# Kernel optimization log

Measured on AMD Instinct MI355X. Metric: run time of the kernel, lower is better.

Reference implementation:

```python
import jax, jax.numpy as jnp
import numpy as np

# tiny-cuda-nn HashGrid config from the module
N_LEVELS = 12
F_PER_LEVEL = 2
LOG2_T = 16
T = 1 << LOG2_T            # 65536 entries per level
BASE_RES = 4
PER_LEVEL_SCALE = 1.61
HASH_PRIME_Y = np.uint32(2654435761)
HIDDEN = 256
OUT = 3
N_POINTS = 1048576

# per-level scale / resolution (tcnn: scale = base*s^l - 1, res = ceil(scale)+1)
_LEVEL_SCALES = [BASE_RES * (PER_LEVEL_SCALE ** l) - 1.0 for l in range(N_LEVELS)]
_LEVEL_RES = [int(np.ceil(s)) + 1 for s in _LEVEL_SCALES]

_CORNERS = np.array([[0, 0], [1, 0], [0, 1], [1, 1]], dtype=np.uint32)  # [4,2]


def hash_encode(x, tables):
    """x: [N,2] in [0,1); tables: [L,T,F]. Returns [N, L*F]."""
    offs_u = jnp.asarray(_CORNERS)                      # [4,2] uint32
    offs_f = offs_u.astype(x.dtype)                     # [4,2]
    feats = []
    for l in range(N_LEVELS):
        s = _LEVEL_SCALES[l]
        res = _LEVEL_RES[l]
        pos = x * jnp.asarray(s, x.dtype) + 0.5         # [N,2]
        p0f = jnp.floor(pos)
        w = pos - p0f                                   # [N,2] frac, differentiable
        p0 = p0f.astype(jnp.uint32)                     # [N,2]
        c = p0[:, None, :] + offs_u[None]               # [N,4,2] corner coords
        # bilinear weight per corner: prod over dims of (w if offset==1 else 1-w)
        wc = jnp.where(offs_f[None] == 1.0, w[:, None, :], 1.0 - w[:, None, :]).prod(-1)  # [N,4]
        if res * res <= T:
            # dense (tight grid) indexing
            cx = jnp.minimum(c[..., 0], np.uint32(res - 1))
            cy = jnp.minimum(c[..., 1], np.uint32(res - 1))
            idx = cx + cy * np.uint32(res)
        else:
            # spatial hash: x*1 XOR y*prime, masked to table size
            idx = (c[..., 0] ^ (c[..., 1] * HASH_PRIME_Y)) & np.uint32(T - 1)
        f = tables[l][idx.astype(jnp.int32)]            # [N,4,F] gather
        feats.append((wc[..., None] * f).sum(axis=1))   # [N,F]
    return jnp.concatenate(feats, axis=-1)              # [N, L*F]


def setup_inputs() -> dict:
    key = jax.random.key(0)
    ks = jax.random.split(key, 10)
    x = jax.random.uniform(ks[0], (N_POINTS, 2), dtype=jnp.float32)
    # tcnn initializes hash tables uniform in [-1e-4, 1e-4]
    tables = jax.random.uniform(ks[1], (N_LEVELS, T, F_PER_LEVEL), dtype=jnp.float32,
                                minval=-1e-4, maxval=1e-4)
    d_in = N_LEVELS * F_PER_LEVEL

    def lin(k, fan_in, fan_out):
        bound = 1.0 / np.sqrt(fan_in)
        kw, kb = jax.random.split(k)
        W = jax.random.uniform(kw, (fan_in, fan_out), dtype=jnp.float32, minval=-bound, maxval=bound)
        b = jax.random.uniform(kb, (fan_out,), dtype=jnp.float32, minval=-bound, maxval=bound)
        return W, b

    W1, b1 = lin(ks[2], d_in, HIDDEN)
    W2, b2 = lin(ks[3], HIDDEN, HIDDEN)
    W3, b3 = lin(ks[4], HIDDEN, HIDDEN)
    Wo, bo = lin(ks[5], HIDDEN, OUT)
    return {"x": x, "tables": tables, "W1": W1, "b1": b1, "W2": W2, "b2": b2,
            "W3": W3, "b3": b3, "Wo": Wo, "bo": bo}


def reference(x, tables, W1, b1, W2, b2, W3, b3, Wo, bo):
    enc = hash_encode(x, tables)                        # [N,24]
    h = jax.nn.relu(enc @ W1 + b1)
    h = jax.nn.relu(h @ W2 + b2)
    h = jax.nn.relu(h @ W3 + b3)
    return h @ Wo + bo                                  # [N,3]
```

## Files before the change

kernel.cpp:

```cpp
#include <hip/hip_runtime.h>

typedef _Float16 f16;
typedef _Float16 f16x2 __attribute__((ext_vector_type(2)));
typedef _Float16 f16x4 __attribute__((ext_vector_type(4)));
typedef _Float16 f16x8 __attribute__((ext_vector_type(8)));
typedef float    f32x4 __attribute__((ext_vector_type(4)));

#define ES 40
#define NPTS 128

__device__ __forceinline__ f16* hswz(f16* base, int p, int fbyte) {
  return (f16*)((char*)base + p * 512 + (fbyte ^ ((p & 7) << 4)));
}
__device__ __forceinline__ const f16* hswz(const f16* base, int p, int fbyte) {
  return (const f16*)((const char*)base + p * 512 + (fbyte ^ ((p & 7) << 4)));
}

static __device__ const float c_scale[12] = {
  3.0f, 5.44f, 9.3684f, 15.693124f, 25.87592964f, 42.2702467204f,
  68.665097219844f, 111.16080652394884f, 179.5788985035576f,
  289.7320265907278f, 467.0785628110717f, 752.6064861258255f };
static __device__ const unsigned c_res[12] = {4,7,11,17,27,44,70,113,181,291,469,754};

__global__ __launch_bounds__(256) void prep_weights(
    const float* __restrict__ W1, const float* __restrict__ W2,
    const float* __restrict__ W3, const float* __restrict__ Wo,
    f16* __restrict__ ws)
{
  int i = blockIdx.x * 256 + threadIdx.x;
  if (i < 8192) {
    int o = i >> 5, k = i & 31;
    ws[i] = (k < 24) ? (f16)W1[k * 256 + o] : (f16)0.0f;
  } else if (i < 73728) {
    int j = i - 8192; int o = j >> 8, k = j & 255;
    ws[i] = (f16)W2[k * 256 + o];
  } else if (i < 139264) {
    int j = i - 73728; int o = j >> 8, k = j & 255;
    ws[i] = (f16)W3[k * 256 + o];
  } else if (i < 143360) {
    int j = i - 139264; int o = j >> 8, k = j & 255;
    ws[i] = (o < 3) ? (f16)Wo[k * 3 + o] : (f16)0.0f;
  }
}

__device__ __forceinline__ void layer256(
    f16* h, const f16* __restrict__ WT,
    const float* __restrict__ bias,
    int w, int l15, int g)
{
  f32x4 acc[4][8];
  #pragma unroll
  for (int mt = 0; mt < 4; ++mt)
    #pragma unroll
    for (int nt = 0; nt < 8; ++nt) acc[mt][nt] = (f32x4)0.0f;

  #pragma unroll
  for (int ks = 0; ks < 8; ++ks) {
    f16x8 a[4], b[8];
    #pragma unroll
    for (int mt = 0; mt < 4; ++mt)
      a[mt] = *(const f16x8*)(WT + (w*64 + mt*16 + l15) * 256 + ks*32 + g*8);
    #pragma unroll
    for (int nt = 0; nt < 8; ++nt)
      b[nt] = *(const f16x8*)hswz(h, nt*16 + l15, ks*64 + g*16);
    #pragma unroll
    for (int mt = 0; mt < 4; ++mt)
      #pragma unroll
      for (int nt = 0; nt < 8; ++nt)
        acc[mt][nt] = __builtin_amdgcn_mfma_f32_16x16x32_f16(a[mt], b[nt], acc[mt][nt], 0, 0, 0);
  }
  __syncthreads();
  #pragma unroll
  for (int mt = 0; mt < 4; ++mt) {
    f32x4 bv = *(const f32x4*)(bias + w*64 + mt*16 + g*4);
    #pragma unroll
    for (int nt = 0; nt < 8; ++nt) {
      f16x4 hv;
      #pragma unroll
      for (int r = 0; r < 4; ++r) {
        float v = acc[mt][nt][r] + bv[r];
        hv[r] = (f16)fmaxf(v, 0.0f);
      }
      *(f16x4*)hswz(h, nt*16 + l15, (w*64 + mt*16 + g*4) * 2) = hv;
    }
  }
  __syncthreads();
}

__global__ __launch_bounds__(256, 2) void hashmlp_kernel(
    const float* __restrict__ x, const float* __restrict__ tables,
    const float* __restrict__ b1, const float* __restrict__ b2,
    const float* __restrict__ b3, const float* __restrict__ bo,
    const f16* __restrict__ ws, float* __restrict__ out)
{
  __shared__ __align__(16) f16 s_enc[NPTS * ES];
  __shared__ __align__(16) f16 s_h[NPTS * 256];

  const int tid = threadIdx.x;
  const int blk = blockIdx.x;

  {
    int p = tid >> 1, sub = tid & 1;
    int gp = blk * NPTS + p;
    float2 xy = ((const float2*)x)[gp];
    #pragma unroll
    for (int j = 0; j < 6; ++j) {
      int l = sub * 6 + j;
      float s = c_scale[l];
      unsigned res = c_res[l];
      float px = __fadd_rn(__fmul_rn(xy.x, s), 0.5f);
      float py = __fadd_rn(__fmul_rn(xy.y, s), 0.5f);
      float fx = floorf(px), fy = floorf(py);
      float wx = px - fx, wy = py - fy;
      unsigned ix = (unsigned)fx, iy = (unsigned)fy;
      unsigned i00, i10, i01, i11;
      if (res * res <= 65536u) {
        unsigned rm = res - 1u;
        unsigned x0 = min(ix, rm), x1 = min(ix + 1u, rm);
        unsigned y0 = min(iy, rm), y1 = min(iy + 1u, rm);
        i00 = x0 + y0 * res; i10 = x1 + y0 * res;
        i01 = x0 + y1 * res; i11 = x1 + y1 * res;
      } else {
        unsigned h0 = iy * 2654435761u, h1 = (iy + 1u) * 2654435761u;
        i00 = (ix ^ h0) & 65535u;  i10 = ((ix + 1u) ^ h0) & 65535u;
        i01 = (ix ^ h1) & 65535u;  i11 = ((ix + 1u) ^ h1) & 65535u;
      }
      const float2* tb = (const float2*)(tables + l * 131072);
      float2 f00 = tb[i00], f10 = tb[i10], f01 = tb[i01], f11 = tb[i11];
      float w00 = (1.f - wx) * (1.f - wy), w10 = wx * (1.f - wy);
      float w01 = (1.f - wx) * wy,         w11 = wx * wy;
      float e0 = w00 * f00.x + w10 * f10.x + w01 * f01.x + w11 * f11.x;
      float e1 = w00 * f00.y + w10 * f10.y + w01 * f01.y + w11 * f11.y;
      f16x2 pk; pk[0] = (f16)e0; pk[1] = (f16)e1;
      *(f16x2*)(&s_enc[p * ES + l * 2]) = pk;
    }
    f16x4 z; z[0] = (f16)0.0f; z[1] = (f16)0.0f; z[2] = (f16)0.0f; z[3] = (f16)0.0f;
    *(f16x4*)(&s_enc[p * ES + 24 + sub * 4]) = z;
  }
  __syncthreads();

  const int w = tid >> 6, lane = tid & 63;
  const int l15 = lane & 15, g = lane >> 4;
  const f16* W1T = ws;
  const f16* W2T = ws + 8192;
  const f16* W3T = ws + 73728;
  const f16* WoT = ws + 139264;

  {
    f32x4 acc[4][8];
    #pragma unroll
    for (int mt = 0; mt < 4; ++mt)
      #pragma unroll
      for (int nt = 0; nt < 8; ++nt) acc[mt][nt] = (f32x4)0.0f;
    f16x8 a[4], b[8];
    #pragma unroll
    for (int mt = 0; mt < 4; ++mt)
      a[mt] = *(const f16x8*)(W1T + (w*64 + mt*16 + l15) * 32 + g*8);
    #pragma unroll
    for (int nt = 0; nt < 8; ++nt)
      b[nt] = *(const f16x8*)(&s_enc[(nt*16 + l15) * ES + g*8]);
    #pragma unroll
    for (int mt = 0; mt < 4; ++mt)
      #pragma unroll
      for (int nt = 0; nt < 8; ++nt)
        acc[mt][nt] = __builtin_amdgcn_mfma_f32_16x16x32_f16(a[mt], b[nt], acc[mt][nt], 0, 0, 0);
    #pragma unroll
    for (int mt = 0; mt < 4; ++mt) {
      f32x4 bv = *(const f32x4*)(b1 + w*64 + mt*16 + g*4);
      #pragma unroll
      for (int nt = 0; nt < 8; ++nt) {
        f16x4 hv;
        #pragma unroll
        for (int r = 0; r < 4; ++r) {
          float v = acc[mt][nt][r] + bv[r];
          hv[r] = (f16)fmaxf(v, 0.0f);
        }
        *(f16x4*)hswz(s_h, nt*16 + l15, (w*64 + mt*16 + g*4) * 2) = hv;
      }
    }
  }
  __syncthreads();

  layer256(s_h, W2T, b2, w, l15, g);
  layer256(s_h, W3T, b3, w, l15, g);

  {
    f32x4 acc0 = (f32x4)0.0f, acc1 = (f32x4)0.0f;
    #pragma unroll
    for (int ks = 0; ks < 8; ++ks) {
      f16x8 a = *(const f16x8*)(WoT + l15 * 256 + ks*32 + g*8);
      f16x8 b0 = *(const f16x8*)hswz(s_h, (2*w+0)*16 + l15, ks*64 + g*16);
      f16x8 b1v = *(const f16x8*)hswz(s_h, (2*w+1)*16 + l15, ks*64 + g*16);
      acc0 = __builtin_amdgcn_mfma_f32_16x16x32_f16(a, b0, acc0, 0, 0, 0);
      acc1 = __builtin_amdgcn_mfma_f32_16x16x32_f16(a, b1v, acc1, 0, 0, 0);
    }
    if (g == 0) {
      int gp0 = blk * NPTS + (2*w+0) * 16 + l15;
      int gp1 = blk * NPTS + (2*w+1) * 16 + l15;
      out[gp0 * 3 + 0] = acc0[0] + bo[0];
      out[gp0 * 3 + 1] = acc0[1] + bo[1];
      out[gp0 * 3 + 2] = acc0[2] + bo[2];
      out[gp1 * 3 + 0] = acc1[0] + bo[0];
      out[gp1 * 3 + 1] = acc1[1] + bo[1];
      out[gp1 * 3 + 2] = acc1[2] + bo[2];
    }
  }
}

extern "C" void kernel_launch(void* const* d_in, const int* in_sizes, int n_in,
                              void* d_out, int out_size, void* d_ws, size_t ws_size,
                              hipStream_t stream) {
  const float* x  = (const float*)d_in[0];
  const float* tb = (const float*)d_in[1];
  const float* W1 = (const float*)d_in[2];
  const float* b1 = (const float*)d_in[3];
  const float* W2 = (const float*)d_in[4];
  const float* b2 = (const float*)d_in[5];
  const float* W3 = (const float*)d_in[6];
  const float* b3 = (const float*)d_in[7];
  const float* Wo = (const float*)d_in[8];
  const float* bo = (const float*)d_in[9];
  f16* ws = (f16*)d_ws;

  prep_weights<<<560, 256, 0, stream>>>(W1, W2, W3, Wo, ws);
  hashmlp_kernel<<<8192, 256, 0, stream>>>(x, tb, b1, b2, b3, bo, ws, (float*)d_out);
}
```

Before: 367.6 us.

## Use two waves per block with 128-row output tiles and bias-initialized accumulators

Cuts the block from 256 to 128 threads (2 waves), so each wave now computes 128 output neurons across 128 points. Each B fragment read from shared memory feeds twice as many MFMAs, which lowers LDS traffic per flop. Bias is folded into the accumulator initialisation, and each thread now encodes all 12 hash levels for one point. The cost is 256 fp32 accumulator registers per thread and half as many waves per CU, which risks spills and less latency hiding for the hash gathers.

```diff
diff --git a/kernel.cpp b/kernel.cpp
--- a/kernel.cpp
+++ b/kernel.cpp
@@ -48,46 +48,45 @@
     const float* __restrict__ bias,
     int w, int l15, int g)
 {
-  f32x4 acc[4][8];
+  f32x4 acc[8][8];
   #pragma unroll
-  for (int mt = 0; mt < 4; ++mt)
-    #pragma unroll
-    for (int nt = 0; nt < 8; ++nt) acc[mt][nt] = (f32x4)0.0f;
+  for (int mt = 0; mt < 8; ++mt) {
+    f32x4 bv = *(const f32x4*)(bias + w*128 + mt*16 + g*4);
+    #pragma unroll
+    for (int nt = 0; nt < 8; ++nt) acc[mt][nt] = bv;
+  }
 
   #pragma unroll
   for (int ks = 0; ks < 8; ++ks) {
-    f16x8 a[4], b[8];
-    #pragma unroll
-    for (int mt = 0; mt < 4; ++mt)
-      a[mt] = *(const f16x8*)(WT + (w*64 + mt*16 + l15) * 256 + ks*32 + g*8);
+    f16x8 a[8], b[8];
+    #pragma unroll
+    for (int mt = 0; mt < 8; ++mt)
+      a[mt] = *(const f16x8*)(WT + (w*128 + mt*16 + l15) * 256 + ks*32 + g*8);
     #pragma unroll
     for (int nt = 0; nt < 8; ++nt)
       b[nt] = *(const f16x8*)hswz(h, nt*16 + l15, ks*64 + g*16);
     #pragma unroll
-    for (int mt = 0; mt < 4; ++mt)
+    for (int mt = 0; mt < 8; ++mt)
       #pragma unroll
       for (int nt = 0; nt < 8; ++nt)
         acc[mt][nt] = __builtin_amdgcn_mfma_f32_16x16x32_f16(a[mt], b[nt], acc[mt][nt], 0, 0, 0);
   }
   __syncthreads();
   #pragma unroll
-  for (int mt = 0; mt < 4; ++mt) {
-    f32x4 bv = *(const f32x4*)(bias + w*64 + mt*16 + g*4);
+  for (int mt = 0; mt < 8; ++mt) {
     #pragma unroll
     for (int nt = 0; nt < 8; ++nt) {
       f16x4 hv;
       #pragma unroll
-      for (int r = 0; r < 4; ++r) {
-        float v = acc[mt][nt][r] + bv[r];
-        hv[r] = (f16)fmaxf(v, 0.0f);
-      }
-      *(f16x4*)hswz(h, nt*16 + l15, (w*64 + mt*16 + g*4) * 2) = hv;
-    }
-  }
-  __syncthreads();
-}
-
-__global__ __launch_bounds__(256, 2) void hashmlp_kernel(
+      for (int r = 0; r < 4; ++r)
+        hv[r] = (f16)fmaxf(acc[mt][nt][r], 0.0f);
+      *(f16x4*)hswz(h, nt*16 + l15, (w*128 + mt*16 + g*4) * 2) = hv;
+    }
+  }
+  __syncthreads();
+}
+
+__global__ __launch_bounds__(128, 1) void hashmlp_kernel(
     const float* __restrict__ x, const float* __restrict__ tables,
     const float* __restrict__ b1, const float* __restrict__ b2,
     const float* __restrict__ b3, const float* __restrict__ bo,
@@ -100,12 +99,11 @@
   const int blk = blockIdx.x;
 
   {
-    int p = tid >> 1, sub = tid & 1;
+    int p = tid;
     int gp = blk * NPTS + p;
     float2 xy = ((const float2*)x)[gp];
     #pragma unroll
-    for (int j = 0; j < 6; ++j) {
-      int l = sub * 6 + j;
+    for (int l = 0; l < 12; ++l) {
       float s = c_scale[l];
       unsigned res = c_res[l];
       float px = __fadd_rn(__fmul_rn(xy.x, s), 0.5f);
@@ -135,7 +133,8 @@
       *(f16x2*)(&s_enc[p * ES + l * 2]) = pk;
     }
     f16x4 z; z[0] = (f16)0.0f; z[1] = (f16)0.0f; z[2] = (f16)0.0f; z[3] = (f16)0.0f;
-    *(f16x4*)(&s_enc[p * ES + 24 + sub * 4]) = z;
+    *(f16x4*)(&s_enc[p * ES + 24]) = z;
+    *(f16x4*)(&s_enc[p * ES + 28]) = z;
   }
   __syncthreads();
 
@@ -147,35 +146,34 @@
   const f16* WoT = ws + 139264;
 
   {
-    f32x4 acc[4][8];
-    #pragma unroll
-    for (int mt = 0; mt < 4; ++mt)
-      #pragma unroll
-      for (int nt = 0; nt < 8; ++nt) acc[mt][nt] = (f32x4)0.0f;
-    f16x8 a[4], b[8];
-    #pragma unroll
-    for (int mt = 0; mt < 4; ++mt)
-      a[mt] = *(const f16x8*)(W1T + (w*64 + mt*16 + l15) * 32 + g*8);
+    f32x4 acc[8][8];
+    #pragma unroll
+    for (int mt = 0; mt < 8; ++mt) {
+      f32x4 bv = *(const f32x4*)(b1 + w*128 + mt*16 + g*4);
+      #pragma unroll
+      for (int nt = 0; nt < 8; ++nt) acc[mt][nt] = bv;
+    }
+    f16x8 a[8], b[8];
+    #pragma unroll
+    for (int mt = 0; mt < 8; ++mt)
+      a[mt] = *(const f16x8*)(W1T + (w*128 + mt*16 + l15) * 32 + g*8);
     #pragma unroll
     for (int nt = 0; nt < 8; ++nt)
       b[nt] = *(const f16x8*)(&s_enc[(nt*16 + l15) * ES + g*8]);
     #pragma unroll
-    for (int mt = 0; mt < 4; ++mt)
+    for (int mt = 0; mt < 8; ++mt)
       #pragma unroll
       for (int nt = 0; nt < 8; ++nt)
         acc[mt][nt] = __builtin_amdgcn_mfma_f32_16x16x32_f16(a[mt], b[nt], acc[mt][nt], 0, 0, 0);
     #pragma unroll
-    for (int mt = 0; mt < 4; ++mt) {
-      f32x4 bv = *(const f32x4*)(b1 + w*64 + mt*16 + g*4);
+    for (int mt = 0; mt < 8; ++mt) {
       #pragma unroll
       for (int nt = 0; nt < 8; ++nt) {
         f16x4 hv;
         #pragma unroll
-        for (int r = 0; r < 4; ++r) {
-          float v = acc[mt][nt][r] + bv[r];
-          hv[r] = (f16)fmaxf(v, 0.0f);
-        }
-        *(f16x4*)hswz(s_h, nt*16 + l15, (w*64 + mt*16 + g*4) * 2) = hv;
+        for (int r = 0; r < 4; ++r)
+          hv[r] = (f16)fmaxf(acc[mt][nt][r], 0.0f);
+        *(f16x4*)hswz(s_h, nt*16 + l15, (w*128 + mt*16 + g*4) * 2) = hv;
       }
     }
   }
@@ -185,24 +183,26 @@
   layer256(s_h, W3T, b3, w, l15, g);
 
   {
-    f32x4 acc0 = (f32x4)0.0f, acc1 = (f32x4)0.0f;
+    f32x4 acc[4];
+    #pragma unroll
+    for (int q = 0; q < 4; ++q) acc[q] = (f32x4)0.0f;
     #pragma unroll
     for (int ks = 0; ks < 8; ++ks) {
       f16x8 a = *(const f16x8*)(WoT + l15 * 256 + ks*32 + g*8);
-      f16x8 b0 = *(const f16x8*)hswz(s_h, (2*w+0)*16 + l15, ks*64 + g*16);
-      f16x8 b1v = *(const f16x8*)hswz(s_h, (2*w+1)*16 + l15, ks*64 + g*16);
-      acc0 = __builtin_amdgcn_mfma_f32_16x16x32_f16(a, b0, acc0, 0, 0, 0);
-      acc1 = __builtin_amdgcn_mfma_f32_16x16x32_f16(a, b1v, acc1, 0, 0, 0);
+      #pragma unroll
+      for (int q = 0; q < 4; ++q) {
+        f16x8 b = *(const f16x8*)hswz(s_h, (w*4+q)*16 + l15, ks*64 + g*16);
+        acc[q] = __builtin_amdgcn_mfma_f32_16x16x32_f16(a, b, acc[q], 0, 0, 0);
+      }
     }
     if (g == 0) {
-      int gp0 = blk * NPTS + (2*w+0) * 16 + l15;
-      int gp1 = blk * NPTS + (2*w+1) * 16 + l15;
-      out[gp0 * 3 + 0] = acc0[0] + bo[0];
-      out[gp0 * 3 + 1] = acc0[1] + bo[1];
-      out[gp0 * 3 + 2] = acc0[2] + bo[2];
-      out[gp1 * 3 + 0] = acc1[0] + bo[0];
-      out[gp1 * 3 + 1] = acc1[1] + bo[1];
-      out[gp1 * 3 + 2] = acc1[2] + bo[2];
+      #pragma unroll
+      for (int q = 0; q < 4; ++q) {
+        int gp = blk * NPTS + (w*4+q) * 16 + l15;
+        out[gp * 3 + 0] = acc[q][0] + bo[0];
+        out[gp * 3 + 1] = acc[q][1] + bo[1];
+        out[gp * 3 + 2] = acc[q][2] + bo[2];
+      }
     }
   }
 }
@@ -223,5 +223,5 @@
   f16* ws = (f16*)d_ws;
 
   prep_weights<<<560, 256, 0, stream>>>(W1, W2, W3, Wo, ws);
-  hashmlp_kernel<<<8192, 256, 0, stream>>>(x, tb, b1, b2, b3, bo, ws, (float*)d_out);
-}
+  hashmlp_kernel<<<8192, 128, 0, stream>>>(x, tb, b1, b2, b3, bo, ws, (float*)d_out);
+}
```

Result: slower. 437.7 us (+19.1%).

## Software-pipeline weight loads across MLP layers and fold bias into accumulators

Applied to the files above, without the earlier changes.

Restructures the MLP layers so global weight fragments are prefetched one to two k-steps ahead through a triple-buffered register ring. The first k-slices of the next layer's weights (and the output layer's weights) are loaded during the tail of the current layer. Bias is loaded up front and used as the initial accumulator value, and the swizzled LDS addresses are precomputed once per thread. This is meant to hide global/L2 latency of weight loads behind MFMA work, at the cost of more live registers, which could spill or reduce occupancy at the 2-block launch bound.

```diff
diff --git a/kernel.cpp b/kernel.cpp
--- a/kernel.cpp
+++ b/kernel.cpp
@@ -9,12 +9,6 @@
 #define ES 40
 #define NPTS 128
 
-__device__ __forceinline__ f16* hswz(f16* base, int p, int fbyte) {
-  return (f16*)((char*)base + p * 512 + (fbyte ^ ((p & 7) << 4)));
-}
-__device__ __forceinline__ const f16* hswz(const f16* base, int p, int fbyte) {
-  return (const f16*)((const char*)base + p * 512 + (fbyte ^ ((p & 7) << 4)));
-}
 
 static __device__ const float c_scale[12] = {
   3.0f, 5.44f, 9.3684f, 15.693124f, 25.87592964f, 42.2702467204f,
@@ -43,45 +37,73 @@
   }
 }
 
-__device__ __forceinline__ void layer256(
-    f16* h, const f16* __restrict__ WT,
-    const float* __restrict__ bias,
-    int w, int l15, int g)
+template<bool NEXT_OUT>
+__device__ __forceinline__ void layer256_pipe(
+    f16* __restrict__ h, const f16* __restrict__ WT,
+    const f32x4* bv, f16x8* cur0, f16x8* cur1,
+    const f16* __restrict__ WTn, const float* __restrict__ bn,
+    f16x8* nxt0, f16x8* nxt1, f32x4* bvn, f16x8* aout,
+    const int* vbase, const int* wbase, int w, int l15, int g)
 {
   f32x4 acc[4][8];
   #pragma unroll
   for (int mt = 0; mt < 4; ++mt)
     #pragma unroll
-    for (int nt = 0; nt < 8; ++nt) acc[mt][nt] = (f32x4)0.0f;
-
+    for (int nt = 0; nt < 8; ++nt) acc[mt][nt] = bv[mt];
+
+  f16x8 abuf[3][4];
+  #pragma unroll
+  for (int mt = 0; mt < 4; ++mt) { abuf[0][mt] = cur0[mt]; abuf[1][mt] = cur1[mt]; }
+
+  const char* hb = (const char*)h;
   #pragma unroll
   for (int ks = 0; ks < 8; ++ks) {
-    f16x8 a[4], b[8];
-    #pragma unroll
-    for (int mt = 0; mt < 4; ++mt)
-      a[mt] = *(const f16x8*)(WT + (w*64 + mt*16 + l15) * 256 + ks*32 + g*8);
-    #pragma unroll
-    for (int nt = 0; nt < 8; ++nt)
-      b[nt] = *(const f16x8*)hswz(h, nt*16 + l15, ks*64 + g*16);
-    #pragma unroll
-    for (int mt = 0; mt < 4; ++mt)
-      #pragma unroll
-      for (int nt = 0; nt < 8; ++nt)
-        acc[mt][nt] = __builtin_amdgcn_mfma_f32_16x16x32_f16(a[mt], b[nt], acc[mt][nt], 0, 0, 0);
+    if (ks < 6) {
+      #pragma unroll
+      for (int mt = 0; mt < 4; ++mt)
+        abuf[(ks+2)%3][mt] = *(const f16x8*)(WT + (w*64 + mt*16 + l15)*256 + (ks+2)*32 + g*8);
+    } else if (ks == 6) {
+      if (NEXT_OUT) {
+        #pragma unroll
+        for (int q = 0; q < 4; ++q)
+          aout[q] = *(const f16x8*)(WTn + l15*256 + q*32 + g*8);
+      } else {
+        #pragma unroll
+        for (int mt = 0; mt < 4; ++mt)
+          nxt0[mt] = *(const f16x8*)(WTn + (w*64 + mt*16 + l15)*256 + g*8);
+        #pragma unroll
+        for (int mt = 0; mt < 4; ++mt)
+          bvn[mt] = *(const f32x4*)(bn + w*64 + mt*16 + g*4);
+      }
+    } else {
+      if (NEXT_OUT) {
+        #pragma unroll
+        for (int q = 0; q < 4; ++q)
+          aout[4+q] = *(const f16x8*)(WTn + l15*256 + (4+q)*32 + g*8);
+      } else {
+        #pragma unroll
+        for (int mt = 0; mt < 4; ++mt)
+          nxt1[mt] = *(const f16x8*)(WTn + (w*64 + mt*16 + l15)*256 + 32 + g*8);
+      }
+    }
+    #pragma unroll
+    for (int nt = 0; nt < 8; ++nt) {
+      f16x8 b = *(const f16x8*)(hb + vbase[ks] + nt*8192);
+      #pragma unroll
+      for (int mt = 0; mt < 4; ++mt)
+        acc[mt][nt] = __builtin_amdgcn_mfma_f32_16x16x32_f16(abuf[ks%3][mt], b, acc[mt][nt], 0, 0, 0);
+    }
   }
   __syncthreads();
   #pragma unroll
   for (int mt = 0; mt < 4; ++mt) {
-    f32x4 bv = *(const f32x4*)(bias + w*64 + mt*16 + g*4);
     #pragma unroll
     for (int nt = 0; nt < 8; ++nt) {
       f16x4 hv;
       #pragma unroll
-      for (int r = 0; r < 4; ++r) {
-        float v = acc[mt][nt][r] + bv[r];
-        hv[r] = (f16)fmaxf(v, 0.0f);
-      }
-      *(f16x4*)hswz(h, nt*16 + l15, (w*64 + mt*16 + g*4) * 2) = hv;
+      for (int r = 0; r < 4; ++r)
+        hv[r] = (f16)fmaxf(acc[mt][nt][r], 0.0f);
+      *(f16x4*)((char*)h + wbase[mt] + nt*8192) = hv;
     }
   }
   __syncthreads();
@@ -98,6 +120,36 @@
 
   const int tid = threadIdx.x;
   const int blk = blockIdx.x;
+  const int w = tid >> 6, lane = tid & 63;
+  const int l15 = lane & 15, g = lane >> 4;
+
+  const f16* W1T = ws;
+  const f16* W2T = ws + 8192;
+  const f16* W3T = ws + 73728;
+  const f16* WoT = ws + 139264;
+
+  f16x8 a1[4], pn0[4], pn1[4];
+  f32x4 bvA[4], bvB[4];
+  #pragma unroll
+  for (int mt = 0; mt < 4; ++mt) {
+    a1[mt]  = *(const f16x8*)(W1T + (w*64 + mt*16 + l15)*32 + g*8);
+    pn0[mt] = *(const f16x8*)(W2T + (w*64 + mt*16 + l15)*256 + g*8);
+    pn1[mt] = *(const f16x8*)(W2T + (w*64 + mt*16 + l15)*256 + 32 + g*8);
+    bvA[mt] = *(const f32x4*)(b1 + w*64 + mt*16 + g*4);
+    bvB[mt] = *(const f32x4*)(b2 + w*64 + mt*16 + g*4);
+  }
+  float bo0 = bo[0], bo1 = bo[1], bo2 = bo[2];
+
+  int vbase[8], wbase[4];
+  {
+    int K = (l15 & 7) << 4;
+    #pragma unroll
+    for (int ks = 0; ks < 8; ++ks)
+      vbase[ks] = l15*512 + ((ks*64 + g*16) ^ K);
+    #pragma unroll
+    for (int mt = 0; mt < 4; ++mt)
+      wbase[mt] = l15*512 + (((w*64 + mt*16 + g*4)*2) ^ K);
+  }
 
   {
     int p = tid >> 1, sub = tid & 1;
@@ -139,70 +191,59 @@
   }
   __syncthreads();
 
-  const int w = tid >> 6, lane = tid & 63;
-  const int l15 = lane & 15, g = lane >> 4;
-  const f16* W1T = ws;
-  const f16* W2T = ws + 8192;
-  const f16* W3T = ws + 73728;
-  const f16* WoT = ws + 139264;
-
   {
     f32x4 acc[4][8];
     #pragma unroll
     for (int mt = 0; mt < 4; ++mt)
       #pragma unroll
-      for (int nt = 0; nt < 8; ++nt) acc[mt][nt] = (f32x4)0.0f;
-    f16x8 a[4], b[8];
-    #pragma unroll
-    for (int mt = 0; mt < 4; ++mt)
-      a[mt] = *(const f16x8*)(W1T + (w*64 + mt*16 + l15) * 32 + g*8);
-    #pragma unroll
-    for (int nt = 0; nt < 8; ++nt)
-      b[nt] = *(const f16x8*)(&s_enc[(nt*16 + l15) * ES + g*8]);
-    #pragma unroll
-    for (int mt = 0; mt < 4; ++mt)
-      #pragma unroll
-      for (int nt = 0; nt < 8; ++nt)
-        acc[mt][nt] = __builtin_amdgcn_mfma_f32_16x16x32_f16(a[mt], b[nt], acc[mt][nt], 0, 0, 0);
+      for (int nt = 0; nt < 8; ++nt) acc[mt][nt] = bvA[mt];
+    #pragma unroll
+    for (int nt = 0; nt < 8; ++nt) {
+      f16x8 b = *(const f16x8*)(&s_enc[(nt*16 + l15) * ES + g*8]);
+      #pragma unroll
+      for (int mt = 0; mt < 4; ++mt)
+        acc[mt][nt] = __builtin_amdgcn_mfma_f32_16x16x32_f16(a1[mt], b, acc[mt][nt], 0, 0, 0);
+    }
     #pragma unroll
     for (int mt = 0; mt < 4; ++mt) {
-      f32x4 bv = *(const f32x4*)(b1 + w*64 + mt*16 + g*4);
       #pragma unroll
       for (int nt = 0; nt < 8; ++nt) {
         f16x4 hv;
         #pragma unroll
-        for (int r = 0; r < 4; ++r) {
-          float v = acc[mt][nt][r] + bv[r];
-          hv[r] = (f16)fmaxf(v, 0.0f);
-        }
-        *(f16x4*)hswz(s_h, nt*16 + l15, (w*64 + mt*16 + g*4) * 2) = hv;
-      }
-    }
-  }
-  __syncthreads();
-
-  layer256(s_h, W2T, b2, w, l15, g);
-  layer256(s_h, W3T, b3, w, l15, g);
+        for (int r = 0; r < 4; ++r)
+          hv[r] = (f16)fmaxf(acc[mt][nt][r], 0.0f);
+        *(f16x4*)((char*)s_h + wbase[mt] + nt*8192) = hv;
+      }
+    }
+  }
+  __syncthreads();
+
+  f16x8 qn0[4], qn1[4], aout[8];
+  f32x4 bvC[4];
+  layer256_pipe<false>(s_h, W2T, bvB, pn0, pn1, W3T, b3, qn0, qn1, bvC, aout,
+                       vbase, wbase, w, l15, g);
+  layer256_pipe<true >(s_h, W3T, bvC, qn0, qn1, WoT, nullptr, pn0, pn1, bvC, aout,
+                       vbase, wbase, w, l15, g);
 
   {
     f32x4 acc0 = (f32x4)0.0f, acc1 = (f32x4)0.0f;
+    const char* hb = (const char*)s_h;
     #pragma unroll
     for (int ks = 0; ks < 8; ++ks) {
-      f16x8 a = *(const f16x8*)(WoT + l15 * 256 + ks*32 + g*8);
-      f16x8 b0 = *(const f16x8*)hswz(s_h, (2*w+0)*16 + l15, ks*64 + g*16);
-      f16x8 b1v = *(const f16x8*)hswz(s_h, (2*w+1)*16 + l15, ks*64 + g*16);
-      acc0 = __builtin_amdgcn_mfma_f32_16x16x32_f16(a, b0, acc0, 0, 0, 0);
-      acc1 = __builtin_amdgcn_mfma_f32_16x16x32_f16(a, b1v, acc1, 0, 0, 0);
+      f16x8 b0 = *(const f16x8*)(hb + vbase[ks] + (2*w+0)*8192);
+      f16x8 b1v = *(const f16x8*)(hb + vbase[ks] + (2*w+1)*8192);
+      acc0 = __builtin_amdgcn_mfma_f32_16x16x32_f16(aout[ks], b0, acc0, 0, 0, 0);
+      acc1 = __builtin_amdgcn_mfma_f32_16x16x32_f16(aout[ks], b1v, acc1, 0, 0, 0);
     }
     if (g == 0) {
       int gp0 = blk * NPTS + (2*w+0) * 16 + l15;
       int gp1 = blk * NPTS + (2*w+1) * 16 + l15;
-      out[gp0 * 3 + 0] = acc0[0] + bo[0];
-      out[gp0 * 3 + 1] = acc0[1] + bo[1];
-      out[gp0 * 3 + 2] = acc0[2] + bo[2];
-      out[gp1 * 3 + 0] = acc1[0] + bo[0];
-      out[gp1 * 3 + 1] = acc1[1] + bo[1];
-      out[gp1 * 3 + 2] = acc1[2] + bo[2];
+      out[gp0 * 3 + 0] = acc0[0] + bo0;
+      out[gp0 * 3 + 1] = acc0[1] + bo1;
+      out[gp0 * 3 + 2] = acc0[2] + bo2;
+      out[gp1 * 3 + 0] = acc1[0] + bo0;
+      out[gp1 * 3 + 1] = acc1[1] + bo1;
+      out[gp1 * 3 + 2] = acc1[2] + bo2;
     }
   }
 }
```

Measured after the change: 365.2 us. About the same (-0.7%).
